# Optimization experiments

Measured on AMD Instinct MI355X. Metric: run time of the kernel, lower is better.

Reference implementation:

```python
import jax, jax.numpy as jnp
import numpy as np

D_MODEL = 1024
N_HEADS = 16
HEAD_DIM = D_MODEL // N_HEADS
NEG_INF = -1e9


def setup_inputs() -> dict:
    key = jax.random.key(0)
    ks = jax.random.split(key, 6)
    B, T, C = 4, 2048, D_MODEL
    x = jax.random.normal(ks[0], (B, T, C), dtype=jnp.float32)
    # causal mask, broadcastable over batch and heads
    mask = jnp.tril(jnp.ones((T, T), dtype=jnp.int32))[None, None]
    scale = 1.0 / np.sqrt(C)
    W_qkv = jax.random.normal(ks[1], (3 * C, C), dtype=jnp.float32) * scale
    b_qkv = jnp.zeros((3 * C,), dtype=jnp.float32)
    W_out = jax.random.normal(ks[2], (C, C), dtype=jnp.float32) * scale
    b_out = jnp.zeros((C,), dtype=jnp.float32)
    return {"x": x, "mask": mask, "W_qkv": W_qkv, "b_qkv": b_qkv,
            "W_out": W_out, "b_out": b_out}


def reference(x, mask, W_qkv, b_qkv, W_out, b_out):
    B, T, C = x.shape
    H, D = N_HEADS, HEAD_DIM
    qkv = x @ W_qkv.T + b_qkv                      # [B, T, 3C]
    q, k, v = jnp.split(qkv, 3, axis=-1)
    # [B, T, C] -> [B, H, T, D]
    q = q.reshape(B, T, H, D).transpose(0, 2, 1, 3)
    k = k.reshape(B, T, H, D).transpose(0, 2, 1, 3)
    v = v.reshape(B, T, H, D).transpose(0, 2, 1, 3)
    scores = jnp.einsum("bhqd,bhkd->bhqk", q, k) / np.sqrt(D)
    scores = jnp.where(mask == 0, NEG_INF, scores)
    att = jax.nn.softmax(scores, axis=-1)          # dropout p=0 (eval)
    out = jnp.einsum("bhqk,bhkd->bhqd", att, v)    # [B, H, T, D]
    out = out.transpose(0, 2, 1, 3).reshape(B, T, C)
    return out @ W_out.T + b_out
```

## Files before the change

### kernel.cpp

```cpp
#include <hip/hip_runtime.h>
#include <hip/hip_bf16.h>

typedef unsigned short u16;
typedef unsigned int u32;
using short8 = __attribute__((ext_vector_type(8))) short;
using f32x4  = __attribute__((ext_vector_type(4))) float;
using f32x16 = __attribute__((ext_vector_type(16))) float;
using uint2v = __attribute__((ext_vector_type(2))) u32;

#define T_SEQ 2048
#define C_DIM 1024
#define NH 16
#define HD 64

#if __has_builtin(__builtin_amdgcn_exp2f)
#define EXP2(x) __builtin_amdgcn_exp2f(x)
#else
#define EXP2(x) exp2f(x)
#endif

__device__ __forceinline__ u16 f2bf(float f) {
    unsigned int u = __float_as_uint(f);
    unsigned int r = (u + 0x7fffu + ((u >> 16) & 1u)) >> 16;
    return (u16)r;
}
__device__ __forceinline__ u32 cvtpk(float lo, float hi) {
    u32 r;
    asm("v_cvt_pk_bf16_f32 %0, %1, %2" : "=v"(r) : "v"(lo), "v"(hi));
    return r;
}
__device__ __forceinline__ short8 mk8(u32 a, u32 b, u32 c, u32 d) {
    union { u32 u[4]; short8 s; } t;
    t.u[0] = a; t.u[1] = b; t.u[2] = c; t.u[3] = d;
    return t.s;
}
__device__ __forceinline__ void gl_lds16(const u16* g, u16* l) {
    __builtin_amdgcn_global_load_lds(
        (const __attribute__((address_space(1))) unsigned int*)g,
        (__attribute__((address_space(3))) unsigned int*)l, 16, 0, 0);
}
template <int N> __device__ __forceinline__ void s_vmcnt();
template <> __device__ __forceinline__ void s_vmcnt<0>() {
    asm volatile("s_waitcnt vmcnt(0)" ::: "memory");
}
template <> __device__ __forceinline__ void s_vmcnt<2>() {
    asm volatile("s_waitcnt vmcnt(2)" ::: "memory");
}
template <> __device__ __forceinline__ void s_vmcnt<4>() {
    asm volatile("s_waitcnt vmcnt(4)" ::: "memory");
}
__device__ __forceinline__ void BAR() {
    asm volatile("" ::: "memory");
    __builtin_amdgcn_s_barrier();
    asm volatile("" ::: "memory");
}

__global__ __launch_bounds__(256) void cvt_f32_bf16(const float* __restrict__ in,
                                                    u16* __restrict__ out, int n8) {
    int i = blockIdx.x * blockDim.x + threadIdx.x;
    if (i >= n8) return;
    const float4* p = (const float4*)in + (size_t)i * 2;
    float4 a = p[0], b = p[1];
    short8 o;
    o[0] = (short)f2bf(a.x); o[1] = (short)f2bf(a.y);
    o[2] = (short)f2bf(a.z); o[3] = (short)f2bf(a.w);
    o[4] = (short)f2bf(b.x); o[5] = (short)f2bf(b.y);
    o[6] = (short)f2bf(b.z); o[7] = (short)f2bf(b.w);
    *(short8*)(out + (size_t)i * 8) = o;
}

__global__ __launch_bounds__(256) void cvt_w2(const float* __restrict__ a,
                                              u16* __restrict__ oa, int na8,
                                              const float* __restrict__ b,
                                              u16* __restrict__ ob, int nb8) {
    int i = blockIdx.x * blockDim.x + threadIdx.x;
    const float* src;
    u16* dst;
    if (i < na8) { src = a; dst = oa; }
    else if (i < na8 + nb8) { src = b; dst = ob; i -= na8; }
    else return;
    const float4* p = (const float4*)src + (size_t)i * 2;
    float4 x = p[0], y = p[1];
    short8 o;
    o[0] = (short)f2bf(x.x); o[1] = (short)f2bf(x.y);
    o[2] = (short)f2bf(x.z); o[3] = (short)f2bf(x.w);
    o[4] = (short)f2bf(y.x); o[5] = (short)f2bf(y.y);
    o[6] = (short)f2bf(y.z); o[7] = (short)f2bf(y.w);
    *(short8*)(dst + (size_t)i * 8) = o;
}

template <int EPI, int NX>
__global__ __launch_bounds__(256) void gemm_bt(const u16* __restrict__ A,
                                               const u16* __restrict__ Bt,
                                               const float* __restrict__ bias,
                                               u16* __restrict__ qb, u16* __restrict__ kb,
                                               u16* __restrict__ vtb, float* __restrict__ Cf,
                                               int M, int N, int K) {
    __shared__ __align__(16) u16 Al[2][128][32];
    __shared__ __align__(16) u16 Bl[2][128][32];
    const int tid = threadIdx.x;
    const int lane = tid & 63, wid = tid >> 6;
    const int li = lane & 15, g = lane >> 4;
    const int wr = (wid >> 1) * 64, wc = (wid & 1) * 64;

    const int bid = blockIdx.x;
    const int xcd = bid & 7;
    const int r_ = bid >> 3;
    const int xq = r_ >> 5;
    const int rem = r_ & 31;
    const int yloc = rem >> 2, xr = rem & 3;
    const size_t m0 = (size_t)(xcd * 8 + yloc) * 128;
    const size_t n0 = (size_t)(xq * 4 + xr) * 128;

    const int srow = lane >> 2;
    const int sch = (lane & 3) ^ ((srow >> 1) & 3);
    const u16* aA = A + (m0 + wid * 32 + srow) * (size_t)K + sch * 8;
    const u16* aB = Bt + (n0 + wid * 32 + srow) * (size_t)K + sch * 8;

    f32x4 acc[4][4] = {};
    const int nt = K / 32;

    auto STAGE = [&](int buf, int k0) {
        gl_lds16(aA + k0, &Al[buf][wid * 32][0]);
        gl_lds16(aA + 16 * (size_t)K + k0, &Al[buf][wid * 32 + 16][0]);
        gl_lds16(aB + k0, &Bl[buf][wid * 32][0]);
        gl_lds16(aB + 16 * (size_t)K + k0, &Bl[buf][wid * 32 + 16][0]);
    };

    STAGE(0, 0);
#pragma unroll 2
    for (int t = 0; t < nt; ++t) {
        if (t + 1 < nt) { STAGE((t + 1) & 1, (t + 1) * 32); s_vmcnt<4>(); }
        else            { s_vmcnt<0>(); }
        BAR();
        short8 af[4], bf[4];
#pragma unroll
        for (int i = 0; i < 4; i++) {
            int row = wr + i * 16 + li;
            af[i] = *(const short8*)&Al[t & 1][row][(g ^ ((row >> 1) & 3)) * 8];
        }
#pragma unroll
        for (int i = 0; i < 4; i++) {
            int row = wc + i * 16 + li;
            bf[i] = *(const short8*)&Bl[t & 1][row][(g ^ ((row >> 1) & 3)) * 8];
        }
        __builtin_amdgcn_s_setprio(1);
#pragma unroll
        for (int mi = 0; mi < 4; mi++)
#pragma unroll
            for (int ni = 0; ni < 4; ni++)
                acc[mi][ni] = __builtin_amdgcn_mfma_f32_16x16x32_bf16(af[mi], bf[ni],
                                                                      acc[mi][ni], 0, 0, 0);
        __builtin_amdgcn_s_setprio(0);
        BAR();
    }

#pragma unroll
    for (int mi = 0; mi < 4; mi++)
#pragma unroll
        for (int ni = 0; ni < 4; ni++) {
            size_t col = n0 + wc + ni * 16 + li;
            size_t row0 = m0 + wr + mi * 16 + g * 4;
            if (EPI == 0) {
                int which = (int)(col >> 10);
                int rem2 = (int)(col & 1023);
                int h = rem2 >> 6, d = rem2 & 63;
                size_t b = row0 >> 11, t0v = row0 & 2047;
                float bv = bias[col];
                if (which == 2) {
                    ushort4 o4;
                    o4.x = f2bf(acc[mi][ni][0] + bv);
                    o4.y = f2bf(acc[mi][ni][1] + bv);
                    o4.z = f2bf(acc[mi][ni][2] + bv);
                    o4.w = f2bf(acc[mi][ni][3] + bv);
                    *(ushort4*)(vtb + (((b * NH) + h) * (size_t)HD + d) * T_SEQ + t0v) = o4;
                } else {
                    u16* dst = (which == 0) ? qb : kb;
                    float sc = (which == 0) ? 0.18033688f : 1.0f;
#pragma unroll
                    for (int r = 0; r < 4; r++)
                        dst[(((b * NH) + h) * T_SEQ + t0v + r) * HD + d] =
                            f2bf((acc[mi][ni][r] + bv) * sc);
                }
            } else {
                float bv = bias[col];
#pragma unroll
                for (int r = 0; r < 4; r++)
                    Cf[(row0 + r) * (size_t)N + col] = acc[mi][ni][r] + bv;
            }
        }
}

__global__ __launch_bounds__(512) void attn_fwd2(const u16* __restrict__ Q,
                                                 const u16* __restrict__ K,
                                                 const u16* __restrict__ Vt,
                                                 u16* __restrict__ O) {
    __shared__ __align__(16) u16 KL[2][64 * 64];
    __shared__ __align__(16) u16 VL[2][64 * 64];
    const int tid = threadIdx.x;
    const int lane = tid & 63, wid = tid >> 6;
    const int l31 = lane & 31, hi = lane >> 5;

    const int wg = blockIdx.x;
    const int j = wg >> 8, c = wg & 255;
    const int xcd = c & 7, m = c >> 3;
    const int bh = (xcd << 3) | (m >> 2);
    const int v = m & 3;
    const int qt = j ? v : (7 - v);

    const size_t bhT = (size_t)bh * T_SEQ;
    const int srow8 = lane >> 3, sch = (lane & 7) ^ srow8;
    const int b = bh >> 4, h = bh & 15;
    const int x7 = l31 & 7;

    const int q0 = qt * 256;
    const int qw0 = q0 + wid * 32;
    const int nkt = 4 * qt + 4;

    short8 qf[4];
    {
        const u16* qp = Q + (bhT + qw0 + l31) * HD + hi * 8;
#pragma unroll
        for (int s = 0; s < 4; s++) qf[s] = *(const short8*)(qp + s * 16);
    }

    f32x16 o0 = {}, o1 = {};
    float l_run = 0.f;

    gl_lds16(K + (bhT + wid * 8 + srow8) * HD + sch * 8, &KL[0][wid * 8 * 64]);
    gl_lds16(Vt + ((size_t)bh * HD + wid * 8 + srow8) * T_SEQ + sch * 8,
             &VL[0][wid * 8 * 64]);

    for (int kt = 0; kt < nkt; kt++) {
        if (kt + 1 < nkt) {
            const int kv0n = (kt + 1) * 64;
            const int nb = (kt + 1) & 1;
            gl_lds16(K + (bhT + kv0n + wid * 8 + srow8) * HD + sch * 8,
                     &KL[nb][wid * 8 * 64]);
            gl_lds16(Vt + ((size_t)bh * HD + wid * 8 + srow8) * T_SEQ + kv0n + sch * 8,
                     &VL[nb][wid * 8 * 64]);
            s_vmcnt<2>();
        } else {
            s_vmcnt<0>();
        }
        BAR();

        const int kv0 = kt * 64;
        if (kv0 <= qw0) {
            const u16* KLb = KL[kt & 1];
            const u16* VLb = VL[kt & 1];

            f32x16 s0 = {}, s1 = {};
            __builtin_amdgcn_s_setprio(1);
#pragma unroll
            for (int sl = 0; sl < 4; sl++) {
                int ch = ((sl * 2 + hi) ^ x7) * 8;
                short8 ka = *(const short8*)&KLb[l31 * 64 + ch];
                s0 = __builtin_amdgcn_mfma_f32_32x32x16_bf16(ka, qf[sl], s0, 0, 0, 0);
                short8 kb2 = *(const short8*)&KLb[(32 + l31) * 64 + ch];
                s1 = __builtin_amdgcn_mfma_f32_32x32x16_bf16(kb2, qf[sl], s1, 0, 0, 0);
            }
            __builtin_amdgcn_s_setprio(0);

            const int qg = qw0 + l31;
            if (kv0 + 63 > qw0) {
#pragma unroll
                for (int r = 0; r < 16; r++) {
                    int kvr = kv0 + (r & 3) + 8 * (r >> 2) + 4 * hi;
                    if (kvr > qg) s0[r] = -1e30f;
                    if (kvr + 32 > qg) s1[r] = -1e30f;
                }
            }

            float ls = 0.f;
#pragma unroll
            for (int r = 0; r < 16; r++) {
                float p = EXP2(s0[r]);
                s0[r] = p; ls += p;
            }
            {
                u32 c0 = cvtpk(s0[0], s0[1]),   c1 = cvtpk(s0[2], s0[3]),
                    c2 = cvtpk(s0[4], s0[5]),   c3 = cvtpk(s0[6], s0[7]),
                    c4 = cvtpk(s0[8], s0[9]),   c5 = cvtpk(s0[10], s0[11]),
                    c6 = cvtpk(s0[12], s0[13]), c7 = cvtpk(s0[14], s0[15]);
                uint2v wA = __builtin_amdgcn_permlane32_swap(c0, c2, false, false);
                uint2v wB = __builtin_amdgcn_permlane32_swap(c1, c3, false, false);
                uint2v wC = __builtin_amdgcn_permlane32_swap(c4, c6, false, false);
                uint2v wD = __builtin_amdgcn_permlane32_swap(c5, c7, false, false);
                short8 paA = mk8(wA[0], wB[0], wA[1], wB[1]);
                short8 paB = mk8(wC[0], wD[0], wC[1], wD[1]);
                __builtin_amdgcn_s_setprio(1);
#pragma unroll
                for (int sl = 0; sl < 2; sl++) {
                    short8 pa = (sl == 0) ? paA : paB;
                    int ch = ((sl * 2 + hi) ^ x7) * 8;
                    short8 va = *(const short8*)&VLb[l31 * 64 + ch];
                    o0 = __builtin_amdgcn_mfma_f32_32x32x16_bf16(pa, va, o0, 0, 0, 0);
                    short8 vb2 = *(const short8*)&VLb[(32 + l31) * 64 + ch];
                    o1 = __builtin_amdgcn_mfma_f32_32x32x16_bf16(pa, vb2, o1, 0, 0, 0);
                }
                __builtin_amdgcn_s_setprio(0);
            }
#pragma unroll
            for (int r = 0; r < 16; r++) {
                float p = EXP2(s1[r]);
                s1[r] = p; ls += p;
            }
            {
                u32 c0 = cvtpk(s1[0], s1[1]),   c1 = cvtpk(s1[2], s1[3]),
                    c2 = cvtpk(s1[4], s1[5]),   c3 = cvtpk(s1[6], s1[7]),
                    c4 = cvtpk(s1[8], s1[9]),   c5 = cvtpk(s1[10], s1[11]),
                    c6 = cvtpk(s1[12], s1[13]), c7 = cvtpk(s1[14], s1[15]);
                uint2v wA = __builtin_amdgcn_permlane32_swap(c0, c2, false, false);
                uint2v wB = __builtin_amdgcn_permlane32_swap(c1, c3, false, false);
                uint2v wC = __builtin_amdgcn_permlane32_swap(c4, c6, false, false);
                uint2v wD = __builtin_amdgcn_permlane32_swap(c5, c7, false, false);
                short8 paC = mk8(wA[0], wB[0], wA[1], wB[1]);
                short8 paD = mk8(wC[0], wD[0], wC[1], wD[1]);
                __builtin_amdgcn_s_setprio(1);
#pragma unroll
                for (int sl = 2; sl < 4; sl++) {
                    short8 pa = (sl == 2) ? paC : paD;
                    int ch = ((sl * 2 + hi) ^ x7) * 8;
                    short8 va = *(const short8*)&VLb[l31 * 64 + ch];
                    o0 = __builtin_amdgcn_mfma_f32_32x32x16_bf16(pa, va, o0, 0, 0, 0);
                    short8 vb2 = *(const short8*)&VLb[(32 + l31) * 64 + ch];
                    o1 = __builtin_amdgcn_mfma_f32_32x32x16_bf16(pa, vb2, o1, 0, 0, 0);
                }
                __builtin_amdgcn_s_setprio(0);
            }
            ls += __shfl_xor(ls, 32);
            l_run += ls;
        }
        BAR();
    }

    const float inv = 1.0f / l_run;
#pragma unroll
    for (int r = 0; r < 16; r++) {
        int qr = (r & 3) + 8 * (r >> 2) + 4 * hi;
        float invr = __shfl(inv, qr);
        int t = q0 + wid * 32 + qr;
        size_t rowoff = ((size_t)b * T_SEQ + t) * C_DIM + h * HD;
        O[rowoff + l31]      = f2bf(o0[r] * invr);
        O[rowoff + 32 + l31] = f2bf(o1[r] * invr);
    }
}

extern "C" void kernel_launch(void* const* d_in, const int* in_sizes, int n_in,
                              void* d_out, int out_size, void* d_ws, size_t ws_size,
                              hipStream_t stream) {
    const float* x     = (const float*)d_in[0];
    const float* W_qkv = (const float*)d_in[2];
    const float* b_qkv = (const float*)d_in[3];
    const float* W_out = (const float*)d_in[4];
    const float* b_out = (const float*)d_in[5];
    float* out = (float*)d_out;

    char* w = (char*)d_ws;
    u16* xb    = (u16*)(w);
    u16* wqkvb = (u16*)(w + 16777216);
    u16* woutb = (u16*)(w + 23068672);
    u16* qb    = (u16*)(w + 25165824);
    u16* kb    = (u16*)(w + 41943040);
    u16* vtb   = (u16*)(w + 58720256);
    u16* attnb = xb;

    cvt_f32_bf16<<<4096, 256, 0, stream>>>(x, xb, 1048576);
    cvt_w2<<<2048, 256, 0, stream>>>(W_qkv, wqkvb, 393216, W_out, woutb, 131072);

    gemm_bt<0, 24><<<1536, 256, 0, stream>>>(xb, wqkvb, b_qkv, qb, kb, vtb, nullptr,
                                             8192, 3072, 1024);

    attn_fwd2<<<512, 512, 0, stream>>>(qb, kb, vtb, attnb);

    gemm_bt<1, 8><<<512, 256, 0, stream>>>(attnb, woutb, b_out, nullptr, nullptr,
                                           nullptr, out, 8192, 1024, 1024);
}
```

Before: 160.3 us.

## Triple-buffer GEMM LDS staging and merge conversion kernels into one launch

The GEMM K-loop moves from double to triple buffering of LDS tiles, prefetching two stages ahead with a matching vmcnt wait, so global-load latency is better hidden behind MFMA work. The loop unroll drops to 1 and the buffer index rotates modulo 3. Separately, the two fp32-to-bf16 conversion kernels become one launch covering x and both weight matrices, removing one kernel launch. LDS use grows from 32KB to 48KB per block, which may lower occupancy.

Measured after the change: 158.6 us, median of 2. Within noise of the previous version (-1.0%).

```diff
diff --git a/kernel.cpp b/kernel.cpp
--- a/kernel.cpp
+++ b/kernel.cpp
@@ -49,43 +49,35 @@
 template <> __device__ __forceinline__ void s_vmcnt<4>() {
     asm volatile("s_waitcnt vmcnt(4)" ::: "memory");
 }
+template <> __device__ __forceinline__ void s_vmcnt<8>() {
+    asm volatile("s_waitcnt vmcnt(8)" ::: "memory");
+}
 __device__ __forceinline__ void BAR() {
     asm volatile("" ::: "memory");
     __builtin_amdgcn_s_barrier();
     asm volatile("" ::: "memory");
 }
 
-__global__ __launch_bounds__(256) void cvt_f32_bf16(const float* __restrict__ in,
-                                                    u16* __restrict__ out, int n8) {
-    int i = blockIdx.x * blockDim.x + threadIdx.x;
-    if (i >= n8) return;
-    const float4* p = (const float4*)in + (size_t)i * 2;
-    float4 a = p[0], b = p[1];
-    short8 o;
-    o[0] = (short)f2bf(a.x); o[1] = (short)f2bf(a.y);
-    o[2] = (short)f2bf(a.z); o[3] = (short)f2bf(a.w);
-    o[4] = (short)f2bf(b.x); o[5] = (short)f2bf(b.y);
-    o[6] = (short)f2bf(b.z); o[7] = (short)f2bf(b.w);
-    *(short8*)(out + (size_t)i * 8) = o;
-}
-
-__global__ __launch_bounds__(256) void cvt_w2(const float* __restrict__ a,
-                                              u16* __restrict__ oa, int na8,
-                                              const float* __restrict__ b,
-                                              u16* __restrict__ ob, int nb8) {
+__global__ __launch_bounds__(256) void cvt_all(const float* __restrict__ x,
+                                               u16* __restrict__ ox, int n0,
+                                               const float* __restrict__ a,
+                                               u16* __restrict__ oa, int n1,
+                                               const float* __restrict__ b,
+                                               u16* __restrict__ ob, int n2) {
     int i = blockIdx.x * blockDim.x + threadIdx.x;
     const float* src;
     u16* dst;
-    if (i < na8) { src = a; dst = oa; }
-    else if (i < na8 + nb8) { src = b; dst = ob; i -= na8; }
+    if (i < n0) { src = x; dst = ox; }
+    else if (i < n0 + n1) { src = a; dst = oa; i -= n0; }
+    else if (i < n0 + n1 + n2) { src = b; dst = ob; i -= n0 + n1; }
     else return;
     const float4* p = (const float4*)src + (size_t)i * 2;
-    float4 x = p[0], y = p[1];
+    float4 u = p[0], v = p[1];
     short8 o;
-    o[0] = (short)f2bf(x.x); o[1] = (short)f2bf(x.y);
-    o[2] = (short)f2bf(x.z); o[3] = (short)f2bf(x.w);
-    o[4] = (short)f2bf(y.x); o[5] = (short)f2bf(y.y);
-    o[6] = (short)f2bf(y.z); o[7] = (short)f2bf(y.w);
+    o[0] = (short)f2bf(u.x); o[1] = (short)f2bf(u.y);
+    o[2] = (short)f2bf(u.z); o[3] = (short)f2bf(u.w);
+    o[4] = (short)f2bf(v.x); o[5] = (short)f2bf(v.y);
+    o[6] = (short)f2bf(v.z); o[7] = (short)f2bf(v.w);
     *(short8*)(dst + (size_t)i * 8) = o;
 }
 
@@ -96,8 +88,8 @@
                                                u16* __restrict__ qb, u16* __restrict__ kb,
                                                u16* __restrict__ vtb, float* __restrict__ Cf,
                                                int M, int N, int K) {
-    __shared__ __align__(16) u16 Al[2][128][32];
-    __shared__ __align__(16) u16 Bl[2][128][32];
+    __shared__ __align__(16) u16 Al[3][128][32];
+    __shared__ __align__(16) u16 Bl[3][128][32];
     const int tid = threadIdx.x;
     const int lane = tid & 63, wid = tid >> 6;
     const int li = lane & 15, g = lane >> 4;
@@ -128,21 +120,30 @@
     };
 
     STAGE(0, 0);
-#pragma unroll 2
+    STAGE(1, 32);
+    int cur = 0;
+#pragma unroll 1
     for (int t = 0; t < nt; ++t) {
-        if (t + 1 < nt) { STAGE((t + 1) & 1, (t + 1) * 32); s_vmcnt<4>(); }
-        else            { s_vmcnt<0>(); }
+        if (t + 2 < nt) {
+            int bs = cur + 2; if (bs >= 3) bs -= 3;
+            STAGE(bs, (t + 2) * 32);
+            s_vmcnt<8>();
+        } else if (t + 1 < nt) {
+            s_vmcnt<4>();
+        } else {
+            s_vmcnt<0>();
+        }
         BAR();
         short8 af[4], bf[4];
 #pragma unroll
         for (int i = 0; i < 4; i++) {
             int row = wr + i * 16 + li;
-            af[i] = *(const short8*)&Al[t & 1][row][(g ^ ((row >> 1) & 3)) * 8];
+            af[i] = *(const short8*)&Al[cur][row][(g ^ ((row >> 1) & 3)) * 8];
         }
 #pragma unroll
         for (int i = 0; i < 4; i++) {
             int row = wc + i * 16 + li;
-            bf[i] = *(const short8*)&Bl[t & 1][row][(g ^ ((row >> 1) & 3)) * 8];
+            bf[i] = *(const short8*)&Bl[cur][row][(g ^ ((row >> 1) & 3)) * 8];
         }
         __builtin_amdgcn_s_setprio(1);
 #pragma unroll
@@ -153,6 +154,7 @@
                                                                       acc[mi][ni], 0, 0, 0);
         __builtin_amdgcn_s_setprio(0);
         BAR();
+        cur = (cur == 2) ? 0 : cur + 1;
     }
 
 #pragma unroll
@@ -366,8 +368,8 @@
     u16* vtb   = (u16*)(w + 58720256);
     u16* attnb = xb;
 
-    cvt_f32_bf16<<<4096, 256, 0, stream>>>(x, xb, 1048576);
-    cvt_w2<<<2048, 256, 0, stream>>>(W_qkv, wqkvb, 393216, W_out, woutb, 131072);
+    cvt_all<<<6144, 256, 0, stream>>>(x, xb, 1048576, W_qkv, wqkvb, 393216,
+                                      W_out, woutb, 131072);
 
     gemm_bt<0, 24><<<1536, 256, 0, stream>>>(xb, wqkvb, b_qkv, qb, kb, vtb, nullptr,
                                              8192, 3072, 1024);
```
